# Performance work log

Hardware: AMD Instinct MI355X
Metric: run time of the kernel (lower is better)

Reference implementation:

```python
import jax, jax.numpy as jnp
import numpy as np

B, S, HID = 2, 2048, 2048
H, D, KV = 16, 128, 4          # heads, head_dim, kv heads
REP = H // KV                  # GQA repeat factor
THETA = 10000.0


def setup_inputs() -> dict:
    key = jax.random.key(0)
    ks = jax.random.split(key, 12)
    query = jax.random.normal(ks[0], (B, S, HID), jnp.float32)
    k_in = jax.random.normal(ks[1], (B, S, HID), jnp.float32)
    v_in = jax.random.normal(ks[2], (B, S, HID), jnp.float32)
    # additive causal mask: 0 on/below diag, -10000 above
    causal = jnp.tril(jnp.ones((S, S), jnp.float32))
    mask = jnp.broadcast_to((1.0 - causal) * -10000.0, (B, 1, S, S))
    # rotary tables (cos/sin of freqs_cis), shape [S, D//2]
    inv_freq = 1.0 / (THETA ** (jnp.arange(0, D, 2, dtype=jnp.float32) / D))
    ang = jnp.outer(jnp.arange(S, dtype=jnp.float32), inv_freq)
    freqs_cos, freqs_sin = jnp.cos(ang), jnp.sin(ang)
    sd = 0.02
    Wq = jax.random.normal(ks[3], (HID, H * D), jnp.float32) * sd
    bq = jnp.zeros((H * D,), jnp.float32)
    Wk = jax.random.normal(ks[4], (HID, KV * D), jnp.float32) * sd
    bk = jnp.zeros((KV * D,), jnp.float32)
    Wv = jax.random.normal(ks[5], (HID, KV * D), jnp.float32) * sd
    bv = jnp.zeros((KV * D,), jnp.float32)
    Wo = jax.random.normal(ks[6], (H * D, HID), jnp.float32) * sd
    bo = jnp.zeros((HID,), jnp.float32)
    return {"query": query, "key": k_in, "value": v_in, "mask": mask,
            "freqs_cos": freqs_cos, "freqs_sin": freqs_sin,
            "Wq": Wq, "bq": bq, "Wk": Wk, "bk": bk,
            "Wv": Wv, "bv": bv, "Wo": Wo, "bo": bo}


def _rope(x, cos, sin):
    # x: [B,S,h,D]; pairs adjacent dims as complex (view_as_complex)
    xr = x.reshape(*x.shape[:-1], D // 2, 2)
    xe, xo = xr[..., 0], xr[..., 1]
    c = cos[None, :, None, :]
    s = sin[None, :, None, :]
    re = xe * c - xo * s
    im = xe * s + xo * c
    return jnp.stack([re, im], axis=-1).reshape(x.shape)


def reference(query, key, value, mask, freqs_cos, freqs_sin,
              Wq, bq, Wk, bk, Wv, bv, Wo, bo):
    q = (query @ Wq + bq).reshape(B, S, H, D)
    k = (key @ Wk + bk).reshape(B, S, KV, D)
    v = (value @ Wv + bv).reshape(B, S, KV, D)
    # repeat_kv: torch.repeat_interleave along head dim
    k = jnp.repeat(k, REP, axis=2)
    v = jnpp_repeat = jnp.repeat(v, REP, axis=2)
    q = _rope(q, freqs_cos, freqs_sin)
    k = _rope(k, freqs_cos, freqs_sin)
    q = q.transpose(0, 2, 1, 3)  # [B,H,S,D]
    k = k.transpose(0, 2, 1, 3)
    v = v.transpose(0, 2, 1, 3)
    scores = jnp.einsum('bhqd,bhkd->bhqk', q, k) / jnp.sqrt(jnp.float32(D))
    scores = scores + mask
    probs = jax.nn.softmax(scores, axis=-1)
    ctx = jnp.einsum('bhqk,bhkd->bhqd', probs, v)
    ctx = ctx.transpose(0, 2, 1, 3).reshape(B, S, H * D)
    return ctx @ Wo + bo
```

## Files before the change

kernel.cpp:

```cpp
#include <hip/hip_runtime.h>
#include <stdint.h>

#define BB 2
#define SS 2048
#define HID 2048
#define NH 16
#define DD 128
#define NKV 4

typedef unsigned short u16;
typedef __attribute__((ext_vector_type(8))) short short8;
typedef __attribute__((ext_vector_type(4))) float f32x4;

#if __has_builtin(__builtin_amdgcn_exp2f)
#define EXP2(x) __builtin_amdgcn_exp2f(x)
#else
#define EXP2(x) exp2f(x)
#endif

__device__ __forceinline__ u16 f2bf(float x) {
    union { float f; unsigned u; } v; v.f = x;
    unsigned u = v.u;
    return (u16)((u + 0x7FFFu + ((u >> 16) & 1u)) >> 16);
}

__device__ __forceinline__ void async_lds16(const void* g, void* l) {
    __builtin_amdgcn_global_load_lds(
        (const __attribute__((address_space(1))) void*)(uintptr_t)g,
        (__attribute__((address_space(3))) void*)(uintptr_t)l,
        16, 0, 0);
}

__global__ __launch_bounds__(256) void k_prep(const float* __restrict__ query,
                                              const float* __restrict__ key,
                                              const float* __restrict__ value,
                                              const float* __restrict__ Wq,
                                              const float* __restrict__ Wk,
                                              const float* __restrict__ Wv,
                                              const float* __restrict__ Wo,
                                              u16* __restrict__ qbf,
                                              u16* __restrict__ kbf,
                                              u16* __restrict__ vbf,
                                              u16* __restrict__ Wt,
                                              u16* __restrict__ Wot) {
    __shared__ float tile[32][33];
    int x = blockIdx.x;
    if (x < 24576) {
        const float* in; u16* out;
        if (x < 8192)       { in = query; out = qbf; }
        else if (x < 16384) { in = key;   out = kbf; x -= 8192; }
        else                { in = value; out = vbf; x -= 16384; }
        const int i = x * 256 + threadIdx.x;
        float4 v = ((const float4*)in)[i];
        uint2 o;
        o.x = (unsigned)f2bf(v.x) | ((unsigned)f2bf(v.y) << 16);
        o.y = (unsigned)f2bf(v.z) | ((unsigned)f2bf(v.w) << 16);
        ((uint2*)out)[i] = o;
        return;
    }
    const int v_ = x - 24576;
    const int ty = v_ / 160;
    const int xt = v_ - ty * 160;
    const float* src; u16* dst; int N, n0;
    if (xt < 64)      { src = Wq; dst = Wt;                          N = 2048; n0 = xt * 32; }
    else if (xt < 80) { src = Wk; dst = Wt + (size_t)2048 * 2048;    N = 512;  n0 = (xt - 64) * 32; }
    else if (xt < 96) { src = Wv; dst = Wt + (size_t)2560 * 2048;    N = 512;  n0 = (xt - 80) * 32; }
    else              { src = Wo; dst = Wot;                         N = 2048; n0 = (xt - 96) * 32; }
    const int k0 = ty * 32;
    const int c = threadIdx.x & 31, r = threadIdx.x >> 5;
#pragma unroll
    for (int i = 0; i < 32; i += 8)
        tile[r + i][c] = src[(size_t)(k0 + r + i) * N + n0 + c];
    __syncthreads();
#pragma unroll
    for (int i = 0; i < 32; i += 8)
        dst[(size_t)(n0 + r + i) * 2048 + k0 + c] = f2bf(tile[c][r + i]);
}

__global__ __launch_bounds__(256) void k_gemm_qkv(const u16* __restrict__ qbf,
                                                  const u16* __restrict__ kbf,
                                                  const u16* __restrict__ vbf,
                                                  const u16* __restrict__ Wt,
                                                  const float* __restrict__ bq,
                                                  const float* __restrict__ bk,
                                                  const float* __restrict__ bv,
                                                  const float* __restrict__ fc,
                                                  const float* __restrict__ fs,
                                                  u16* __restrict__ qro,
                                                  u16* __restrict__ kro,
                                                  u16* __restrict__ vtr) {
    __shared__ u16 As[128 * 32];
    __shared__ u16 Bs[128 * 32];
    __shared__ float Ep[4 * 64 * 20];

    const int tid = threadIdx.x;
    const int lane = tid & 63, wave = tid >> 6;
    const int bn = blockIdx.x;
    const int bm = blockIdx.y * 128;
    const u16* A = (bn < 16) ? qbf : (bn < 20) ? kbf : vbf;

    const int srow = tid >> 2, spos = tid & 3;
    const int c0 = (spos ^ ((srow >> 1) & 3)) * 8;
    const u16* gA0 = A  + (size_t)(bm + srow) * 2048 + c0;
    const u16* gA1 = A  + (size_t)(bm + 64 + srow) * 2048 + c0;
    const u16* gB0 = Wt + (size_t)(bn * 128 + srow) * 2048 + c0;
    const u16* gB1 = Wt + (size_t)(bn * 128 + 64 + srow) * 2048 + c0;

    const int r = lane & 15, q4 = lane >> 4;
    const int wm = (wave & 1) * 64, wn = (wave >> 1) * 64;

    int aoff[4], boff[4];
#pragma unroll
    for (int i = 0; i < 4; i++) {
        const int ar = wm + i * 16 + r;
        aoff[i] = ar * 32 + ((q4 ^ ((ar >> 1) & 3)) << 3);
        const int br = wn + i * 16 + r;
        boff[i] = br * 32 + ((q4 ^ ((br >> 1) & 3)) << 3);
    }

    f32x4 acc[4][4] = {};

    for (int kb = 0; kb < 2048; kb += 32) {
        async_lds16(gA0, As + wave * 512);
        async_lds16(gA1, As + 2048 + wave * 512);
        async_lds16(gB0, Bs + wave * 512);
        async_lds16(gB1, Bs + 2048 + wave * 512);
        gA0 += 32; gA1 += 32; gB0 += 32; gB1 += 32;
        __syncthreads();

        short8 av[4], bv_[4];
#pragma unroll
        for (int i = 0; i < 4; i++) av[i] = *(const short8*)(As + aoff[i]);
#pragma unroll
        for (int j = 0; j < 4; j++) bv_[j] = *(const short8*)(Bs + boff[j]);
#pragma unroll
        for (int i = 0; i < 4; i++)
#pragma unroll
            for (int j = 0; j < 4; j++)
                acc[i][j] = __builtin_amdgcn_mfma_f32_16x16x32_bf16(av[i], bv_[j], acc[i][j], 0, 0, 0);
        __syncthreads();
    }

    if (bn < 20) {
        const bool isQ = (bn < 16);
        const float qsc = isQ ? 0.08838834764831845f * 1.4426950408889634f : 1.0f;
        const float* bias = isQ ? bq : bk;
        const int head = isQ ? bn : (bn - 16);
        u16* base = isQ ? qro : kro;
        const int nheads = isQ ? NH : NKV;

        float* ep = Ep + wave * 1280;
        const int rowg = bm + wm + lane;
        const int s = rowg & 2047, bidx = rowg >> 11;
        const float* fcp0 = fc + s * 64;
        const float* fsp0 = fs + s * 64;

#pragma unroll
        for (int j = 0; j < 4; j++) {
            const float bcol = bias[head * 128 + wn + j * 16 + r];
#pragma unroll
            for (int i = 0; i < 4; i++)
#pragma unroll
                for (int g = 0; g < 4; g++)
                    ep[(i * 16 + q4 * 4 + g) * 20 + r] = acc[i][j][g] + bcol;
            float4 x0 = *(float4*)(ep + lane * 20 + 0);
            float4 x1 = *(float4*)(ep + lane * 20 + 4);
            float4 x2 = *(float4*)(ep + lane * 20 + 8);
            float4 x3 = *(float4*)(ep + lane * 20 + 12);
            const int d0 = wn + j * 16;
            const int ii0 = d0 >> 1;
            float4 ca = *(const float4*)(fcp0 + ii0);
            float4 cb = *(const float4*)(fcp0 + ii0 + 4);
            float4 sa = *(const float4*)(fsp0 + ii0);
            float4 sb = *(const float4*)(fsp0 + ii0 + 4);
            float o[16];
            o[0]  = (x0.x * ca.x - x0.y * sa.x) * qsc;  o[1]  = (x0.x * sa.x + x0.y * ca.x) * qsc;
            o[2]  = (x0.z * ca.y - x0.w * sa.y) * qsc;  o[3]  = (x0.z * sa.y + x0.w * ca.y) * qsc;
            o[4]  = (x1.x * ca.z - x1.y * sa.z) * qsc;  o[5]  = (x1.x * sa.z + x1.y * ca.z) * qsc;
            o[6]  = (x1.z * ca.w - x1.w * sa.w) * qsc;  o[7]  = (x1.z * sa.w + x1.w * ca.w) * qsc;
            o[8]  = (x2.x * cb.x - x2.y * sb.x) * qsc;  o[9]  = (x2.x * sb.x + x2.y * cb.x) * qsc;
            o[10] = (x2.z * cb.y - x2.w * sb.y) * qsc;  o[11] = (x2.z * sb.y + x2.w * cb.y) * qsc;
            o[12] = (x3.x * cb.z - x3.y * sb.z) * qsc;  o[13] = (x3.x * sb.z + x3.y * cb.z) * qsc;
            o[14] = (x3.z * cb.w - x3.w * sb.w) * qsc;  o[15] = (x3.z * sb.w + x3.w * cb.w) * qsc;
            uint4 pk;
            pk.x = (unsigned)f2bf(o[0])  | ((unsigned)f2bf(o[1])  << 16) ;
            pk.x |= 0u;
            pk.x = (unsigned)f2bf(o[0])  | ((unsigned)f2bf(o[1])  << 16);
            unsigned w1 = (unsigned)f2bf(o[2])  | ((unsigned)f2bf(o[3])  << 16);
            unsigned w2 = (unsigned)f2bf(o[4])  | ((unsigned)f2bf(o[5])  << 16);
            unsigned w3 = (unsigned)f2bf(o[6])  | ((unsigned)f2bf(o[7])  << 16);
            unsigned w4 = (unsigned)f2bf(o[8])  | ((unsigned)f2bf(o[9])  << 16);
            unsigned w5 = (unsigned)f2bf(o[10]) | ((unsigned)f2bf(o[11]) << 16);
            unsigned w6 = (unsigned)f2bf(o[12]) | ((unsigned)f2bf(o[13]) << 16);
            unsigned w7 = (unsigned)f2bf(o[14]) | ((unsigned)f2bf(o[15]) << 16);
            uint4 lo_ = make_uint4(pk.x, w1, w2, w3);
            uint4 hi_ = make_uint4(w4, w5, w6, w7);
            u16* dst = base + (((size_t)(bidx * nheads + head) * SS + s) << 7) + d0;
            *(uint4*)dst = lo_;
            *(uint4*)(dst + 8) = hi_;
        }
    } else {
#pragma unroll
        for (int j = 0; j < 4; j++) {
            const int col = bn * 128 + wn + j * 16 + r - 2560;
            const int d = col & 127, kv = col >> 7;
            const float bb = bv[col];
#pragma unroll
            for (int i = 0; i < 4; i++) {
                const int row0 = bm + wm + i * 16 + q4 * 4;
                const int s0 = row0 & 2047, b = row0 >> 11;
                uint2 o;
                o.x = (unsigned)f2bf(acc[i][j][0] + bb) | ((unsigned)f2bf(acc[i][j][1] + bb) << 16);
                o.y = (unsigned)f2bf(acc[i][j][2] + bb) | ((unsigned)f2bf(acc[i][j][3] + bb) << 16);
                *(uint2*)(vtr + ((size_t)(b * NKV + kv) * DD + d) * SS + s0) = o;
            }
        }
    }
}

__global__ __launch_bounds__(256) void k_gemm_bt(const u16* __restrict__ A,
                                                 const u16* __restrict__ Bt,
                                                 const float* __restrict__ bias,
                                                 float* __restrict__ C,
                                                 int M, int N, int K) {
    __shared__ u16 As[128 * 32];
    __shared__ u16 Bs[128 * 32];

    const int tid = threadIdx.x;
    const int lane = tid & 63, wave = tid >> 6;
    const int bm = blockIdx.y * 128, bn = blockIdx.x * 128;

    const int srow = tid >> 2, spos = tid & 3;
    const int c0 = (spos ^ ((srow >> 1) & 3)) * 8;
    const u16* gA0 = A  + (size_t)(bm + srow) * K + c0;
    const u16* gA1 = A  + (size_t)(bm + 64 + srow) * K + c0;
    const u16* gB0 = Bt + (size_t)(bn + srow) * K + c0;
    const u16* gB1 = Bt + (size_t)(bn + 64 + srow) * K + c0;

    const int r = lane & 15, q4 = lane >> 4;
    const int wm = (wave & 1) * 64, wn = (wave >> 1) * 64;

    int aoff[4], boff[4];
#pragma unroll
    for (int i = 0; i < 4; i++) {
        const int ar = wm + i * 16 + r;
        aoff[i] = ar * 32 + ((q4 ^ ((ar >> 1) & 3)) << 3);
        const int br = wn + i * 16 + r;
        boff[i] = br * 32 + ((q4 ^ ((br >> 1) & 3)) << 3);
    }

    f32x4 acc[4][4] = {};

    for (int kb = 0; kb < K; kb += 32) {
        async_lds16(gA0, As + wave * 512);
        async_lds16(gA1, As + 2048 + wave * 512);
        async_lds16(gB0, Bs + wave * 512);
        async_lds16(gB1, Bs + 2048 + wave * 512);
        gA0 += 32; gA1 += 32; gB0 += 32; gB1 += 32;
        __syncthreads();

        short8 av[4], bv_[4];
#pragma unroll
        for (int i = 0; i < 4; i++) av[i] = *(const short8*)(As + aoff[i]);
#pragma unroll
        for (int j = 0; j < 4; j++) bv_[j] = *(const short8*)(Bs + boff[j]);
#pragma unroll
        for (int i = 0; i < 4; i++)
#pragma unroll
            for (int j = 0; j < 4; j++)
                acc[i][j] = __builtin_amdgcn_mfma_f32_16x16x32_bf16(av[i], bv_[j], acc[i][j], 0, 0, 0);
        __syncthreads();
    }

#pragma unroll
    for (int j = 0; j < 4; j++) {
        const int col = bn + wn + j * 16 + r;
        const float bb = bias[col];
#pragma unroll
        for (int i = 0; i < 4; i++) {
            const int row = bm + wm + i * 16 + q4 * 4;
#pragma unroll
            for (int g = 0; g < 4; g++)
                C[(size_t)(row + g) * N + col] = acc[i][j][g] + bb;
        }
    }
}

__global__ __launch_bounds__(256) void k_attn(const u16* __restrict__ Q,
                                              const u16* __restrict__ K_,
                                              const u16* __restrict__ V_,
                                              u16* __restrict__ Ctx) {
    __shared__ u16 Ks[32 * 128];
    __shared__ u16 Vs[128 * 32];
    __shared__ u16 Pb[4 * 32 * 40];

    const int tid = threadIdx.x;
    const int lane = tid & 63, wave = tid >> 6;
    const int bh = blockIdx.x;
    const int b = bh >> 4, h = bh & 15;
    const int kvh = (b << 2) | (h >> 2);
    const int qb = (gridDim.y - 1 - blockIdx.y) * 128;
    const int qcol = lane & 15, q4 = lane >> 4;
    const int qw = qb + wave * 32;

    const u16* Qg = Q + ((size_t)bh * SS + qw + qcol) * DD;
    short8 qfr[2][4];
#pragma unroll
    for (int qi = 0; qi < 2; qi++)
#pragma unroll
        for (int c = 0; c < 4; c++)
            qfr[qi][c] = *(const short8*)(Qg + qi * 16 * DD + c * 32 + q4 * 8);

    const u16* Kg = K_ + (size_t)kvh * SS * DD;
    const u16* Vg = V_ + (size_t)kvh * DD * SS;

    const int krow = tid >> 4;
    const int kchunk = (tid & 15) ^ (krow & 7);
    const int vd = tid >> 2;
    const int vchunk = (tid & 3) ^ ((vd >> 1) & 3);

    f32x4 lacc[2] = {};
    f32x4 oacc[2][8] = {};

    const short8 ones = {0x3F80, 0x3F80, 0x3F80, 0x3F80, 0x3F80, 0x3F80, 0x3F80, 0x3F80};
    u16* pb = Pb + wave * 1280;
    unsigned* pb32 = (unsigned*)pb;

    for (int kb = 0; kb < qb + 128; kb += 32) {
        async_lds16(Kg + (size_t)(kb + krow) * DD + kchunk * 8,       Ks + wave * 512);
        async_lds16(Kg + (size_t)(kb + 16 + krow) * DD + kchunk * 8,  Ks + 2048 + wave * 512);
        async_lds16(Vg + (size_t)vd * SS + kb + vchunk * 8,           Vs + wave * 512);
        async_lds16(Vg + (size_t)(vd + 64) * SS + kb + vchunk * 8,    Vs + 2048 + wave * 512);
        __syncthreads();

        if (kb <= qw + 31) {
            f32x4 sc[2][2] = {};
#pragma unroll
            for (int kt = 0; kt < 2; kt++) {
                const int kr = kt * 16 + qcol;
#pragma unroll
                for (int c = 0; c < 4; c++) {
                    short8 kf = *(const short8*)(Ks + kr * 128 + (((c * 4 + q4) ^ (kr & 7)) << 3));
                    sc[kt][0] = __builtin_amdgcn_mfma_f32_16x16x32_bf16(kf, qfr[0][c], sc[kt][0], 0, 0, 0);
                    sc[kt][1] = __builtin_amdgcn_mfma_f32_16x16x32_bf16(kf, qfr[1][c], sc[kt][1], 0, 0, 0);
                }
            }

            if (kb + 32 > qw) {
#pragma unroll
                for (int kt = 0; kt < 2; kt++)
#pragma unroll
                    for (int qi = 0; qi < 2; qi++)
#pragma unroll
                        for (int g = 0; g < 4; g++) {
                            const int key = kb + kt * 16 + q4 * 4 + g;
                            if (key > qw + qi * 16 + qcol) sc[kt][qi][g] = -1e30f;
                        }
            }

            const unsigned sel = 0x07060302u;
#pragma unroll
            for (int qi = 0; qi < 2; qi++) {
                float p0 = EXP2(sc[0][qi][0]), p1 = EXP2(sc[0][qi][1]);
                float p2 = EXP2(sc[0][qi][2]), p3 = EXP2(sc[0][qi][3]);
                float p4 = EXP2(sc[1][qi][0]), p5 = EXP2(sc[1][qi][1]);
                float p6 = EXP2(sc[1][qi][2]), p7 = EXP2(sc[1][qi][3]);
                unsigned pk0 = __builtin_amdgcn_perm(__float_as_uint(p1), __float_as_uint(p0), sel);
                unsigned pk1 = __builtin_amdgcn_perm(__float_as_uint(p3), __float_as_uint(p2), sel);
                unsigned pk2 = __builtin_amdgcn_perm(__float_as_uint(p5), __float_as_uint(p4), sel);
                unsigned pk3 = __builtin_amdgcn_perm(__float_as_uint(p7), __float_as_uint(p6), sel);
                const int row = qi * 16 + qcol;
                *(uint2*)(pb32 + row * 20 + 2 * q4)     = make_uint2(pk0, pk1);
                *(uint2*)(pb32 + row * 20 + 8 + 2 * q4) = make_uint2(pk2, pk3);
            }

            short8 pf0 = *(const short8*)(pb + qcol * 40 + q4 * 8);
            short8 pf1 = *(const short8*)(pb + (16 + qcol) * 40 + q4 * 8);

            lacc[0] = __builtin_amdgcn_mfma_f32_16x16x32_bf16(ones, pf0, lacc[0], 0, 0, 0);
            lacc[1] = __builtin_amdgcn_mfma_f32_16x16x32_bf16(ones, pf1, lacc[1], 0, 0, 0);
#pragma unroll
            for (int dt = 0; dt < 8; dt++) {
                const int vr = dt * 16 + qcol;
                short8 vfr = *(const short8*)(Vs + vr * 32 + ((q4 ^ ((vr >> 1) & 3)) << 3));
                oacc[0][dt] = __builtin_amdgcn_mfma_f32_16x16x32_bf16(vfr, pf0, oacc[0][dt], 0, 0, 0);
                oacc[1][dt] = __builtin_amdgcn_mfma_f32_16x16x32_bf16(vfr, pf1, oacc[1][dt], 0, 0, 0);
            }
        }
        __syncthreads();
    }

#pragma unroll
    for (int qi = 0; qi < 2; qi++) {
        const float inv = 1.0f / lacc[qi][0];
        u16* outp = Ctx + ((size_t)b * SS + qw + qi * 16 + qcol) * (NH * DD) + h * DD;
#pragma unroll
        for (int dt = 0; dt < 8; dt++) {
            unsigned lo = (unsigned)f2bf(oacc[qi][dt][0] * inv) | ((unsigned)f2bf(oacc[qi][dt][1] * inv) << 16);
            unsigned hi = (unsigned)f2bf(oacc[qi][dt][2] * inv) | ((unsigned)f2bf(oacc[qi][dt][3] * inv) << 16);
            *(uint2*)(outp + dt * 16 + q4 * 4) = make_uint2(lo, hi);
        }
    }
}

extern "C" void kernel_launch(void* const* d_in, const int* in_sizes, int n_in,
                              void* d_out, int out_size, void* d_ws, size_t ws_size,
                              hipStream_t stream) {
    const float* query = (const float*)d_in[0];
    const float* key   = (const float*)d_in[1];
    const float* value = (const float*)d_in[2];
    const float* fc    = (const float*)d_in[4];
    const float* fs    = (const float*)d_in[5];
    const float* Wq    = (const float*)d_in[6];
    const float* bq    = (const float*)d_in[7];
    const float* Wk    = (const float*)d_in[8];
    const float* bk    = (const float*)d_in[9];
    const float* Wv    = (const float*)d_in[10];
    const float* bv    = (const float*)d_in[11];
    const float* Wo    = (const float*)d_in[12];
    const float* bo    = (const float*)d_in[13];
    float* out = (float*)d_out;

    char* w = (char*)d_ws;
    u16* qbf = (u16*)(w);
    u16* kbf = (u16*)(w + 16777216);
    u16* vbf = (u16*)(w + 33554432);
    u16* Wt  = (u16*)(w + 50331648);
    u16* Wot = (u16*)(w + 62914560);
    u16* qro = (u16*)(w + 71303168);
    u16* kro = (u16*)(w + 88080384);
    u16* vtr = (u16*)(w + 92274688);
    u16* ctx = (u16*)(w + 96468992);

    k_prep<<<34816, 256, 0, stream>>>(query, key, value, Wq, Wk, Wv, Wo,
                                      qbf, kbf, vbf, Wt, Wot);
    k_gemm_qkv<<<dim3(24, 32), 256, 0, stream>>>(qbf, kbf, vbf, Wt, bq, bk, bv,
                                                 fc, fs, qro, kro, vtr);
    k_attn<<<dim3(32, 16), 256, 0, stream>>>(qro, kro, vtr, ctx);
    k_gemm_bt<<<dim3(16, 32), 256, 0, stream>>>(ctx, Wot, bo, out, 4096, 2048, 2048);
}
```

Baseline: 421.1 us.

## Fuse fp32-to-bf16 activation conversion into QKV GEMM with double-buffered register-staged loads

The separate pass that converted query/key/value activations to bf16 in k_prep is removed. k_gemm_qkv now reads fp32 directly, truncates to bf16 with a byte permute, and writes to LDS. Both GEMMs switch from async global-to-LDS loads to register-staged double-buffered LDS tiles, so the next tile's global loads overlap the current MFMA work. This removes a full read/write pass over the activations, but the GEMM now loads twice as many bytes for A and rounds by truncation instead of round-to-nearest.

```diff
diff --git a/kernel.cpp b/kernel.cpp
--- a/kernel.cpp
+++ b/kernel.cpp
@@ -24,41 +24,18 @@
     return (u16)((u + 0x7FFFu + ((u >> 16) & 1u)) >> 16);
 }
 
-__device__ __forceinline__ void async_lds16(const void* g, void* l) {
-    __builtin_amdgcn_global_load_lds(
-        (const __attribute__((address_space(1))) void*)(uintptr_t)g,
-        (__attribute__((address_space(3))) void*)(uintptr_t)l,
-        16, 0, 0);
-}
-
-__global__ __launch_bounds__(256) void k_prep(const float* __restrict__ query,
-                                              const float* __restrict__ key,
-                                              const float* __restrict__ value,
-                                              const float* __restrict__ Wq,
+__device__ __forceinline__ unsigned pkbf(float lo, float hi) {
+    return __builtin_amdgcn_perm(__float_as_uint(hi), __float_as_uint(lo), 0x07060302u);
+}
+
+__global__ __launch_bounds__(256) void k_prep(const float* __restrict__ Wq,
                                               const float* __restrict__ Wk,
                                               const float* __restrict__ Wv,
                                               const float* __restrict__ Wo,
-                                              u16* __restrict__ qbf,
-                                              u16* __restrict__ kbf,
-                                              u16* __restrict__ vbf,
                                               u16* __restrict__ Wt,
                                               u16* __restrict__ Wot) {
     __shared__ float tile[32][33];
-    int x = blockIdx.x;
-    if (x < 24576) {
-        const float* in; u16* out;
-        if (x < 8192)       { in = query; out = qbf; }
-        else if (x < 16384) { in = key;   out = kbf; x -= 8192; }
-        else                { in = value; out = vbf; x -= 16384; }
-        const int i = x * 256 + threadIdx.x;
-        float4 v = ((const float4*)in)[i];
-        uint2 o;
-        o.x = (unsigned)f2bf(v.x) | ((unsigned)f2bf(v.y) << 16);
-        o.y = (unsigned)f2bf(v.z) | ((unsigned)f2bf(v.w) << 16);
-        ((uint2*)out)[i] = o;
-        return;
-    }
-    const int v_ = x - 24576;
+    const int v_ = blockIdx.x;
     const int ty = v_ / 160;
     const int xt = v_ - ty * 160;
     const float* src; u16* dst; int N, n0;
@@ -77,9 +54,9 @@
         dst[(size_t)(n0 + r + i) * 2048 + k0 + c] = f2bf(tile[c][r + i]);
 }
 
-__global__ __launch_bounds__(256) void k_gemm_qkv(const u16* __restrict__ qbf,
-                                                  const u16* __restrict__ kbf,
-                                                  const u16* __restrict__ vbf,
+__global__ __launch_bounds__(256) void k_gemm_qkv(const float* __restrict__ qf32,
+                                                  const float* __restrict__ kf32,
+                                                  const float* __restrict__ vf32,
                                                   const u16* __restrict__ Wt,
                                                   const float* __restrict__ bq,
                                                   const float* __restrict__ bk,
@@ -89,22 +66,26 @@
                                                   u16* __restrict__ qro,
                                                   u16* __restrict__ kro,
                                                   u16* __restrict__ vtr) {
-    __shared__ u16 As[128 * 32];
-    __shared__ u16 Bs[128 * 32];
-    __shared__ float Ep[4 * 64 * 20];
+    __shared__ char smem[32768];
+    u16* As = (u16*)smem;
+    u16* Bs = (u16*)(smem + 16384);
+    float* Ep = (float*)smem;
 
     const int tid = threadIdx.x;
     const int lane = tid & 63, wave = tid >> 6;
     const int bn = blockIdx.x;
     const int bm = blockIdx.y * 128;
-    const u16* A = (bn < 16) ? qbf : (bn < 20) ? kbf : vbf;
+    const float* A = (bn < 16) ? qf32 : (bn < 20) ? kf32 : vf32;
 
     const int srow = tid >> 2, spos = tid & 3;
-    const int c0 = (spos ^ ((srow >> 1) & 3)) * 8;
-    const u16* gA0 = A  + (size_t)(bm + srow) * 2048 + c0;
-    const u16* gA1 = A  + (size_t)(bm + 64 + srow) * 2048 + c0;
+    const int swz = (srow >> 1) & 3;
+    const int c0 = (spos ^ swz) * 8;
+    const float* gA0 = A + (size_t)(bm + srow) * 2048 + c0;
+    const float* gA1 = gA0 + (size_t)64 * 2048;
     const u16* gB0 = Wt + (size_t)(bn * 128 + srow) * 2048 + c0;
-    const u16* gB1 = Wt + (size_t)(bn * 128 + 64 + srow) * 2048 + c0;
+    const u16* gB1 = gB0 + (size_t)64 * 2048;
+    const int wo0 = srow * 32 + spos * 8;
+    const int wo1 = wo0 + 64 * 32;
 
     const int r = lane & 15, q4 = lane >> 4;
     const int wm = (wave & 1) * 64, wn = (wave >> 1) * 64;
@@ -120,24 +101,52 @@
 
     f32x4 acc[4][4] = {};
 
-    for (int kb = 0; kb < 2048; kb += 32) {
-        async_lds16(gA0, As + wave * 512);
-        async_lds16(gA1, As + 2048 + wave * 512);
-        async_lds16(gB0, Bs + wave * 512);
-        async_lds16(gB1, Bs + 2048 + wave * 512);
-        gA0 += 32; gA1 += 32; gB0 += 32; gB1 += 32;
-        __syncthreads();
-
+    {
+        float4 a00 = *(const float4*)(gA0), a01 = *(const float4*)(gA0 + 4);
+        float4 a10 = *(const float4*)(gA1), a11 = *(const float4*)(gA1 + 4);
+        uint4 b0 = *(const uint4*)(gB0), b1 = *(const uint4*)(gB1);
+        uint4 pa0 = make_uint4(pkbf(a00.x, a00.y), pkbf(a00.z, a00.w), pkbf(a01.x, a01.y), pkbf(a01.z, a01.w));
+        uint4 pa1 = make_uint4(pkbf(a10.x, a10.y), pkbf(a10.z, a10.w), pkbf(a11.x, a11.y), pkbf(a11.z, a11.w));
+        *(uint4*)(As + wo0) = pa0;
+        *(uint4*)(As + wo1) = pa1;
+        *(uint4*)(Bs + wo0) = b0;
+        *(uint4*)(Bs + wo1) = b1;
+    }
+    __syncthreads();
+
+    for (int i = 0; i < 64; i++) {
+        const int par = i & 1;
+        float4 a00, a01, a10, a11; uint4 b0, b1;
+        if (i < 63) {
+            gA0 += 32; gA1 += 32; gB0 += 32; gB1 += 32;
+            a00 = *(const float4*)(gA0); a01 = *(const float4*)(gA0 + 4);
+            a10 = *(const float4*)(gA1); a11 = *(const float4*)(gA1 + 4);
+            b0 = *(const uint4*)(gB0);   b1 = *(const uint4*)(gB1);
+        }
+
+        const u16* Ab = As + par * 4096;
+        const u16* Bb = Bs + par * 4096;
         short8 av[4], bv_[4];
 #pragma unroll
-        for (int i = 0; i < 4; i++) av[i] = *(const short8*)(As + aoff[i]);
-#pragma unroll
-        for (int j = 0; j < 4; j++) bv_[j] = *(const short8*)(Bs + boff[j]);
-#pragma unroll
-        for (int i = 0; i < 4; i++)
+        for (int k = 0; k < 4; k++) av[k] = *(const short8*)(Ab + aoff[k]);
+#pragma unroll
+        for (int k = 0; k < 4; k++) bv_[k] = *(const short8*)(Bb + boff[k]);
+#pragma unroll
+        for (int k = 0; k < 4; k++)
 #pragma unroll
             for (int j = 0; j < 4; j++)
-                acc[i][j] = __builtin_amdgcn_mfma_f32_16x16x32_bf16(av[i], bv_[j], acc[i][j], 0, 0, 0);
+                acc[k][j] = __builtin_amdgcn_mfma_f32_16x16x32_bf16(av[k], bv_[j], acc[k][j], 0, 0, 0);
+
+        if (i < 63) {
+            u16* Aw = As + (par ^ 1) * 4096;
+            u16* Bw = Bs + (par ^ 1) * 4096;
+            uint4 pa0 = make_uint4(pkbf(a00.x, a00.y), pkbf(a00.z, a00.w), pkbf(a01.x, a01.y), pkbf(a01.z, a01.w));
+            uint4 pa1 = make_uint4(pkbf(a10.x, a10.y), pkbf(a10.z, a10.w), pkbf(a11.x, a11.y), pkbf(a11.z, a11.w));
+            *(uint4*)(Aw + wo0) = pa0;
+            *(uint4*)(Aw + wo1) = pa1;
+            *(uint4*)(Bw + wo0) = b0;
+            *(uint4*)(Bw + wo1) = b1;
+        }
         __syncthreads();
     }
 
@@ -182,10 +191,7 @@
             o[10] = (x2.z * cb.y - x2.w * sb.y) * qsc;  o[11] = (x2.z * sb.y + x2.w * cb.y) * qsc;
             o[12] = (x3.x * cb.z - x3.y * sb.z) * qsc;  o[13] = (x3.x * sb.z + x3.y * cb.z) * qsc;
             o[14] = (x3.z * cb.w - x3.w * sb.w) * qsc;  o[15] = (x3.z * sb.w + x3.w * cb.w) * qsc;
-            uint4 pk;
-            pk.x = (unsigned)f2bf(o[0])  | ((unsigned)f2bf(o[1])  << 16) ;
-            pk.x |= 0u;
-            pk.x = (unsigned)f2bf(o[0])  | ((unsigned)f2bf(o[1])  << 16);
+            unsigned w0 = (unsigned)f2bf(o[0])  | ((unsigned)f2bf(o[1])  << 16);
             unsigned w1 = (unsigned)f2bf(o[2])  | ((unsigned)f2bf(o[3])  << 16);
             unsigned w2 = (unsigned)f2bf(o[4])  | ((unsigned)f2bf(o[5])  << 16);
             unsigned w3 = (unsigned)f2bf(o[6])  | ((unsigned)f2bf(o[7])  << 16);
@@ -193,11 +199,9 @@
             unsigned w5 = (unsigned)f2bf(o[10]) | ((unsigned)f2bf(o[11]) << 16);
             unsigned w6 = (unsigned)f2bf(o[12]) | ((unsigned)f2bf(o[13]) << 16);
             unsigned w7 = (unsigned)f2bf(o[14]) | ((unsigned)f2bf(o[15]) << 16);
-            uint4 lo_ = make_uint4(pk.x, w1, w2, w3);
-            uint4 hi_ = make_uint4(w4, w5, w6, w7);
             u16* dst = base + (((size_t)(bidx * nheads + head) * SS + s) << 7) + d0;
-            *(uint4*)dst = lo_;
-            *(uint4*)(dst + 8) = hi_;
+            *(uint4*)dst = make_uint4(w0, w1, w2, w3);
+            *(uint4*)(dst + 8) = make_uint4(w4, w5, w6, w7);
         }
     } else {
 #pragma unroll
@@ -223,19 +227,23 @@
                                                  const float* __restrict__ bias,
                                                  float* __restrict__ C,
                                                  int M, int N, int K) {
-    __shared__ u16 As[128 * 32];
-    __shared__ u16 Bs[128 * 32];
+    __shared__ char smem[32768];
+    u16* As = (u16*)smem;
+    u16* Bs = (u16*)(smem + 16384);
 
     const int tid = threadIdx.x;
     const int lane = tid & 63, wave = tid >> 6;
     const int bm = blockIdx.y * 128, bn = blockIdx.x * 128;
 
     const int srow = tid >> 2, spos = tid & 3;
-    const int c0 = (spos ^ ((srow >> 1) & 3)) * 8;
-    const u16* gA0 = A  + (size_t)(bm + srow) * K + c0;
-    const u16* gA1 = A  + (size_t)(bm + 64 + srow) * K + c0;
+    const int swz = (srow >> 1) & 3;
+    const int c0 = (spos ^ swz) * 8;
+    const u16* gA0 = A + (size_t)(bm + srow) * K + c0;
+    const u16* gA1 = gA0 + (size_t)64 * K;
     const u16* gB0 = Bt + (size_t)(bn + srow) * K + c0;
-    const u16* gB1 = Bt + (size_t)(bn + 64 + srow) * K + c0;
+    const u16* gB1 = gB0 + (size_t)64 * K;
+    const int wo0 = srow * 32 + spos * 8;
+    const int wo1 = wo0 + 64 * 32;
 
     const int r = lane & 15, q4 = lane >> 4;
     const int wm = (wave & 1) * 64, wn = (wave >> 1) * 64;
@@ -251,24 +259,47 @@
 
     f32x4 acc[4][4] = {};
 
-    for (int kb = 0; kb < K; kb += 32) {
-        async_lds16(gA0, As + wave * 512);
-        async_lds16(gA1, As + 2048 + wave * 512);
-        async_lds16(gB0, Bs + wave * 512);
-        async_lds16(gB1, Bs + 2048 + wave * 512);
-        gA0 += 32; gA1 += 32; gB0 += 32; gB1 += 32;
-        __syncthreads();
-
+    {
+        uint4 a0 = *(const uint4*)(gA0), a1 = *(const uint4*)(gA1);
+        uint4 b0 = *(const uint4*)(gB0), b1 = *(const uint4*)(gB1);
+        *(uint4*)(As + wo0) = a0;
+        *(uint4*)(As + wo1) = a1;
+        *(uint4*)(Bs + wo0) = b0;
+        *(uint4*)(Bs + wo1) = b1;
+    }
+    __syncthreads();
+
+    const int iters = K / 32;
+    for (int i = 0; i < iters; i++) {
+        const int par = i & 1;
+        uint4 a0, a1, b0, b1;
+        if (i < iters - 1) {
+            gA0 += 32; gA1 += 32; gB0 += 32; gB1 += 32;
+            a0 = *(const uint4*)(gA0); a1 = *(const uint4*)(gA1);
+            b0 = *(const uint4*)(gB0); b1 = *(const uint4*)(gB1);
+        }
+
+        const u16* Ab = As + par * 4096;
+        const u16* Bb = Bs + par * 4096;
         short8 av[4], bv_[4];
 #pragma unroll
-        for (int i = 0; i < 4; i++) av[i] = *(const short8*)(As + aoff[i]);
-#pragma unroll
-        for (int j = 0; j < 4; j++) bv_[j] = *(const short8*)(Bs + boff[j]);
-#pragma unroll
-        for (int i = 0; i < 4; i++)
+        for (int k = 0; k < 4; k++) av[k] = *(const short8*)(Ab + aoff[k]);
+#pragma unroll
+        for (int k = 0; k < 4; k++) bv_[k] = *(const short8*)(Bb + boff[k]);
+#pragma unroll
+        for (int k = 0; k < 4; k++)
 #pragma unroll
             for (int j = 0; j < 4; j++)
-                acc[i][j] = __builtin_amdgcn_mfma_f32_16x16x32_bf16(av[i], bv_[j], acc[i][j], 0, 0, 0);
+                acc[k][j] = __builtin_amdgcn_mfma_f32_16x16x32_bf16(av[k], bv_[j], acc[k][j], 0, 0, 0);
+
+        if (i < iters - 1) {
+            u16* Aw = As + (par ^ 1) * 4096;
+            u16* Bw = Bs + (par ^ 1) * 4096;
+            *(uint4*)(Aw + wo0) = a0;
+            *(uint4*)(Aw + wo1) = a1;
+            *(uint4*)(Bw + wo0) = b0;
+            *(uint4*)(Bw + wo1) = b1;
+        }
         __syncthreads();
     }
 
@@ -327,10 +358,18 @@
     unsigned* pb32 = (unsigned*)pb;
 
     for (int kb = 0; kb < qb + 128; kb += 32) {
-        async_lds16(Kg + (size_t)(kb + krow) * DD + kchunk * 8,       Ks + wave * 512);
-        async_lds16(Kg + (size_t)(kb + 16 + krow) * DD + kchunk * 8,  Ks + 2048 + wave * 512);
-        async_lds16(Vg + (size_t)vd * SS + kb + vchunk * 8,           Vs + wave * 512);
-        async_lds16(Vg + (size_t)(vd + 64) * SS + kb + vchunk * 8,    Vs + 2048 + wave * 512);
+        __builtin_amdgcn_global_load_lds(
+            (const __attribute__((address_space(1))) void*)(uintptr_t)(Kg + (size_t)(kb + krow) * DD + kchunk * 8),
+            (__attribute__((address_space(3))) void*)(uintptr_t)(Ks + wave * 512), 16, 0, 0);
+        __builtin_amdgcn_global_load_lds(
+            (const __attribute__((address_space(1))) void*)(uintptr_t)(Kg + (size_t)(kb + 16 + krow) * DD + kchunk * 8),
+            (__attribute__((address_space(3))) void*)(uintptr_t)(Ks + 2048 + wave * 512), 16, 0, 0);
+        __builtin_amdgcn_global_load_lds(
+            (const __attribute__((address_space(1))) void*)(uintptr_t)(Vg + (size_t)vd * SS + kb + vchunk * 8),
+            (__attribute__((address_space(3))) void*)(uintptr_t)(Vs + wave * 512), 16, 0, 0);
+        __builtin_amdgcn_global_load_lds(
+            (const __attribute__((address_space(1))) void*)(uintptr_t)(Vg + (size_t)(vd + 64) * SS + kb + vchunk * 8),
+            (__attribute__((address_space(3))) void*)(uintptr_t)(Vs + 2048 + wave * 512), 16, 0, 0);
         __syncthreads();
 
         if (kb <= qw + 31) {
@@ -422,19 +461,15 @@
     float* out = (float*)d_out;
 
     char* w = (char*)d_ws;
-    u16* qbf = (u16*)(w);
-    u16* kbf = (u16*)(w + 16777216);
-    u16* vbf = (u16*)(w + 33554432);
-    u16* Wt  = (u16*)(w + 50331648);
-    u16* Wot = (u16*)(w + 62914560);
-    u16* qro = (u16*)(w + 71303168);
-    u16* kro = (u16*)(w + 88080384);
-    u16* vtr = (u16*)(w + 92274688);
-    u16* ctx = (u16*)(w + 96468992);
-
-    k_prep<<<34816, 256, 0, stream>>>(query, key, value, Wq, Wk, Wv, Wo,
-                                      qbf, kbf, vbf, Wt, Wot);
-    k_gemm_qkv<<<dim3(24, 32), 256, 0, stream>>>(qbf, kbf, vbf, Wt, bq, bk, bv,
+    u16* Wt  = (u16*)(w);
+    u16* Wot = (u16*)(w + 12582912);
+    u16* qro = (u16*)(w + 20971520);
+    u16* kro = (u16*)(w + 37748736);
+    u16* vtr = (u16*)(w + 41943040);
+    u16* ctx = (u16*)(w + 46137344);
+
+    k_prep<<<10240, 256, 0, stream>>>(Wq, Wk, Wv, Wo, Wt, Wot);
+    k_gemm_qkv<<<dim3(24, 32), 256, 0, stream>>>(query, key, value, Wt, bq, bk, bv,
                                                  fc, fs, qro, kro, vtr);
     k_attn<<<dim3(32, 16), 256, 0, stream>>>(qro, kro, vtr, ctx);
     k_gemm_bt<<<dim3(16, 32), 256, 0, stream>>>(ctx, Wot, bo, out, 4096, 2048, 2048);
```

Measured after the change: 444.1 us. +5.5%, slower.
